# Optimization experiments

Hardware: AMD Instinct MI355X
Metric: run time of the kernel (lower is better)

The kernel has to match this reference:

```python
import jax, jax.numpy as jnp
import numpy as np

NUM_HEADS = 16
EPS = 1e-5


def setup_inputs() -> dict:
    key = jax.random.key(0)
    ks = jax.random.split(key, 9)
    B, S, D = 2, 2048, 1024
    s = 1.0 / np.sqrt(D)
    return {
        "x": jax.random.normal(ks[0], (B, S, D), dtype=jnp.float32),
        "Wq": jax.random.uniform(ks[1], (D, D), jnp.float32, -s, s),
        "bq": jax.random.uniform(ks[2], (D,), jnp.float32, -s, s),
        "Wk": jax.random.uniform(ks[3], (D, D), jnp.float32, -s, s),
        "bk": jax.random.uniform(ks[4], (D,), jnp.float32, -s, s),
        "Wv": jax.random.uniform(ks[5], (D, D), jnp.float32, -s, s),
        "bv": jax.random.uniform(ks[6], (D,), jnp.float32, -s, s),
        "Wo": jax.random.uniform(ks[7], (D, D), jnp.float32, -s, s),
        "bo": jax.random.uniform(ks[8], (D,), jnp.float32, -s, s),
    }


def reference(x, Wq, bq, Wk, bk, Wv, bv, Wo, bo):
    B, S, D = x.shape
    H = NUM_HEADS
    hd = D // H
    # projections -> [B, H, S, hd]
    def proj(W, b):
        return (x @ W + b).reshape(B, S, H, hd).transpose(0, 2, 1, 3)
    Q = proj(Wq, bq)
    K = proj(Wk, bk)
    V = proj(Wv, bv)
    scores = jnp.einsum("bhqd,bhkd->bhqk", Q, K) / jnp.sqrt(jnp.float32(hd))
    attn = jax.nn.softmax(scores, axis=-1)  # dropout is identity in eval mode
    out = jnp.einsum("bhqk,bhkd->bhqd", attn, V)
    out = out.transpose(0, 2, 1, 3).reshape(B, S, D)
    out = jax.nn.relu(out @ Wo + bo)
    mu = jnp.mean(out, axis=-1, keepdims=True)
    var = jnp.var(out, axis=-1, keepdims=True)
    return (out - mu) * jax.lax.rsqrt(var + EPS)
```

## Files before the change

kernel.cpp:

```cpp
#include <hip/hip_runtime.h>
#include <hip/hip_bf16.h>
#include <math.h>

#define Bb 2
#define Ss 2048
#define Dd 1024
#define Hh 16
#define HD 64
#define Mm (Bb*Ss)

typedef __attribute__((ext_vector_type(8))) short bf8_t;
typedef __attribute__((ext_vector_type(4))) float f4_t;
typedef __attribute__((ext_vector_type(4))) unsigned u4_t;
typedef __attribute__((ext_vector_type(2))) unsigned uint2v;

#define LOG2E 1.4426950408889634f

#define AS1 __attribute__((address_space(1)))
#define AS3 __attribute__((address_space(3)))

__device__ __forceinline__ void gl2lds16(const void* g, void* l) {
    __builtin_amdgcn_global_load_lds((const AS1 unsigned int*)g,
                                     (AS3 unsigned int*)l, 16, 0, 0);
}
__device__ __forceinline__ short bfr(float f) {
    __hip_bfloat16 h = __float2bfloat16(f);
    return *reinterpret_cast<short*>(&h);
}
__device__ __forceinline__ unsigned pkbf16(float a, float b) {
    const unsigned ua = __builtin_bit_cast(unsigned, a) + 0x8000u;
    const unsigned ub = __builtin_bit_cast(unsigned, b) + 0x8000u;
    return __builtin_amdgcn_perm(ub, ua, 0x07060302u);
}
__device__ __forceinline__ float fexp2(float x) {
    return __builtin_amdgcn_exp2f(x);
}
__device__ __forceinline__ float b2f(unsigned short u) {
    return __builtin_bit_cast(float, (unsigned)u << 16);
}
__device__ __forceinline__ void pl32(unsigned &a, unsigned &b) {
#if __has_builtin(__builtin_amdgcn_permlane32_swap)
    uint2v r = __builtin_amdgcn_permlane32_swap(a, b, false, false);
    a = r[0]; b = r[1];
#else
    asm volatile("v_permlane32_swap_b32 %0, %1" : "+v"(a), "+v"(b));
#endif
}
__device__ __forceinline__ void pl16(unsigned &a, unsigned &b) {
#if __has_builtin(__builtin_amdgcn_permlane16_swap)
    uint2v r = __builtin_amdgcn_permlane16_swap(a, b, false, false);
    a = r[0]; b = r[1];
#else
    asm volatile("v_permlane16_swap_b32 %0, %1" : "+v"(a), "+v"(b));
#endif
}

__global__ __launch_bounds__(256)
void prep(const float* __restrict__ x,
          const float* __restrict__ w0, const float* __restrict__ w1,
          const float* __restrict__ w2, const float* __restrict__ w3,
          __hip_bfloat16* __restrict__ Wt4, __hip_bfloat16* __restrict__ Xh)
{
    const int z = blockIdx.z;
    if (z < 4) {
        const float* W = (z == 0) ? w0 : (z == 1) ? w1 : (z == 2) ? w2 : w3;
        __hip_bfloat16* Wt = Wt4 + (size_t)z * Dd * Dd;
        __shared__ float t[32][33];
        const int n0 = blockIdx.x * 32, k0 = blockIdx.y * 32;
        const int tx = threadIdx.x & 31, ty = threadIdx.x >> 5;
        #pragma unroll
        for (int rr = 0; rr < 4; ++rr)
            t[ty + rr*8][tx] = W[(size_t)(k0 + ty + rr*8) * Dd + n0 + tx];
        __syncthreads();
        #pragma unroll
        for (int rr = 0; rr < 4; ++rr)
            Wt[(size_t)(n0 + ty + rr*8) * Dd + k0 + tx] =
                __float2bfloat16(t[tx][ty + rr*8]);
    } else {
        const int bid = (z - 4) * 1024 + blockIdx.y * 32 + blockIdx.x;
        const size_t i = ((size_t)bid * 256 + threadIdx.x) * 8;
        const float4 a = *(const float4*)&x[i];
        const float4 b = *(const float4*)&x[i + 4];
        bf8_t o;
        o[0] = bfr(a.x); o[1] = bfr(a.y); o[2] = bfr(a.z); o[3] = bfr(a.w);
        o[4] = bfr(b.x); o[5] = bfr(b.y); o[6] = bfr(b.z); o[7] = bfr(b.w);
        *(bf8_t*)&Xh[i] = o;
    }
}

__global__ __launch_bounds__(256)
void gemm_qkv(const __hip_bfloat16* __restrict__ A,
              const __hip_bfloat16* __restrict__ Bt,
              const float* __restrict__ b0, const float* __restrict__ b1,
              const float* __restrict__ b2,
              __hip_bfloat16* __restrict__ Qh, __hip_bfloat16* __restrict__ Kh,
              __hip_bfloat16* __restrict__ Vt)
{
    __shared__ __align__(16) char pool[34816];
    __hip_bfloat16* As = (__hip_bfloat16*)pool;
    __hip_bfloat16* Bs = As + 2 * 128 * 32;

    const int lin  = blockIdx.y * 24 + blockIdx.x;
    const int xcd  = lin & 7;
    const int idx  = lin >> 3;
    const int by   = (xcd >> 1) * 8 + idx / 12;
    const int bx   = (xcd & 1) * 12 + idx % 12;

    const int tid  = threadIdx.x;
    const int wave = tid >> 6;
    const int lane = tid & 63;
    const int llo  = lane & 15;
    const int lhi  = lane >> 4;
    const int wm   = wave & 1;
    const int wn   = wave >> 1;
    const int row0 = by * 128;
    const int col0 = bx * 128;

    size_t aoff[2], boff[2];
    int    loff[2];
    #pragma unroll
    for (int p = 0; p < 2; ++p) {
        const int g = p * 256 + wave * 64 + lane;
        const int r = g >> 2;
        const int kc = ((g & 3) ^ ((r >> 1) & 3)) * 8;
        aoff[p] = (size_t)(row0 + r) * Dd + kc;
        boff[p] = (size_t)(col0 + r) * Dd + kc;
        loff[p] = (p * 256 + wave * 64) * 16;
    }
    const __hip_bfloat16* Acur = A;
    const __hip_bfloat16* Bcur = Bt;

    auto stage = [&](int buf) {
        #pragma unroll
        for (int p = 0; p < 2; ++p) {
            gl2lds16(Acur + aoff[p], (char*)As + buf*8192 + loff[p]);
            gl2lds16(Bcur + boff[p], (char*)Bs + buf*8192 + loff[p]);
        }
        Acur += 32; Bcur += 32;
    };

    const int xch = (lhi ^ ((llo >> 1) & 3)) * 8;

    f4_t acc[4][4] = {};
    stage(0);
    for (int kt = 0; kt < 32; ++kt) {
        const int buf = kt & 1;
        __syncthreads();
        if (kt + 1 < 32) stage(buf ^ 1);

        bf8_t a[4], b[4];
        #pragma unroll
        for (int i = 0; i < 4; ++i)
            a[i] = *(const bf8_t*)&As[buf*4096 + (wm*64 + i*16 + llo) * 32 + xch];
        #pragma unroll
        for (int j = 0; j < 4; ++j)
            b[j] = *(const bf8_t*)&Bs[buf*4096 + (wn*64 + j*16 + llo) * 32 + xch];
        #pragma unroll
        for (int i = 0; i < 4; ++i)
            #pragma unroll
            for (int j = 0; j < 4; ++j)
                acc[i][j] = __builtin_amdgcn_mfma_f32_16x16x32_bf16(
                    a[i], b[j], acc[i][j], 0, 0, 0);
    }

    const int sel   = col0 >> 10;
    const int cbase = col0 & 1023;
    __hip_bfloat16* Ls = (__hip_bfloat16*)pool;
    __syncthreads();

    float bv[4];
    const float* bp = (sel == 0) ? b0 : (sel == 1) ? b1 : b2;
    #pragma unroll
    for (int j = 0; j < 4; ++j) bv[j] = bp[cbase + wn*64 + j*16 + llo];
    const float scale = (sel == 0) ? 0.125f * LOG2E : 1.0f;

    if (sel < 2) {
        #pragma unroll
        for (int i = 0; i < 4; ++i)
            #pragma unroll
            for (int r = 0; r < 4; ++r) {
                const int ml = wm*64 + i*16 + lhi*4 + r;
                #pragma unroll
                for (int j = 0; j < 4; ++j)
                    Ls[ml*136 + wn*64 + j*16 + llo] =
                        __float2bfloat16((acc[i][j][r] + bv[j]) * scale);
            }
        __syncthreads();
        __hip_bfloat16* outQK = (sel == 0) ? Qh : Kh;
        #pragma unroll
        for (int p = 0; p < 8; ++p) {
            const int id = p*256 + tid;
            const int rl = id >> 4;
            const int c8 = (id & 15) * 8;
            const bf8_t v = *(const bf8_t*)&Ls[rl*136 + c8];
            const int m  = row0 + rl;
            const int b_ = m >> 11, s_ = m & (Ss - 1);
            const int col = cbase + c8;
            *(bf8_t*)&outQK[((size_t)(b_*Hh + (col >> 6))*Ss + s_)*HD + (col & 63)] = v;
        }
    } else {
        #pragma unroll
        for (int i = 0; i < 4; ++i)
            #pragma unroll
            for (int r = 0; r < 4; ++r) {
                const int ml = wm*64 + i*16 + lhi*4 + r;
                #pragma unroll
                for (int j = 0; j < 4; ++j)
                    Ls[(wn*64 + j*16 + llo)*136 + ml] =
                        __float2bfloat16(acc[i][j][r] + bv[j]);
            }
        __syncthreads();
        const int b_ = row0 >> 11;
        const int sb = row0 & (Ss - 1);
        #pragma unroll
        for (int p = 0; p < 8; ++p) {
            const int cl = p*16 + (tid >> 4);
            const int m  = (tid & 15) * 8;
            const bf8_t v = *(const bf8_t*)&Ls[cl*136 + m];
            const int cc = cbase + cl;
            *(bf8_t*)&Vt[((size_t)(b_*Hh + (cc >> 6))*HD + (cc & 63))*Ss + sb + m] = v;
        }
    }
}

__global__ __launch_bounds__(256, 2)
void attn_mfma(const __hip_bfloat16* __restrict__ Qh,
               const __hip_bfloat16* __restrict__ Kh,
               const __hip_bfloat16* __restrict__ Vt,
               __hip_bfloat16* __restrict__ Ah)
{
    const int lin  = (blockIdx.z * Hh + blockIdx.y) * (Ss/128) + blockIdx.x;
    const int xcd  = lin & 7;
    const int slot = lin >> 3;
    const int grp  = (xcd << 2) | (slot >> 4);
    const int qc   = slot & 15;
    const int b    = grp >> 4;
    const int h    = grp & 15;

    const int wave = threadIdx.x >> 6;
    const int lane = threadIdx.x & 63;
    const int llo  = lane & 15;
    const int lhi  = lane >> 4;
    const int qb   = qc * 128 + wave * 32;

    const size_t base = ((size_t)(b*Hh + h)) * Ss * HD;

    __shared__ __hip_bfloat16 Ks[2][2 * 64 * 32];
    __shared__ __hip_bfloat16 Vs[2][2 * 64 * 32];

    int koff[2], voff[2], loff[2];
    #pragma unroll
    for (int it = 0; it < 2; ++it) {
        const int g  = it*256 + wave*64 + lane;
        const int hf = g >> 8;
        const int rr = (g >> 2) & 63;
        const int c8 = ((g & 3) ^ ((rr >> 1) & 3)) * 8;
        koff[it] = rr*HD + hf*32 + c8;
        voff[it] = rr*Ss + hf*32 + c8;
        loff[it] = (it*256 + wave*64) * 16;
    }
    const __hip_bfloat16* Kcur = Kh + base;
    const __hip_bfloat16* Vcur = Vt + base;

    auto stage = [&](int buf) {
        #pragma unroll
        for (int it = 0; it < 2; ++it) {
            gl2lds16(Kcur + koff[it], (char*)&Ks[buf][0] + loff[it]);
            gl2lds16(Vcur + voff[it], (char*)&Vs[buf][0] + loff[it]);
        }
        Kcur += 64 * HD;
        Vcur += 64;
    };

    bf8_t qf[2][2];
    #pragma unroll
    for (int s = 0; s < 2; ++s)
        #pragma unroll
        for (int d = 0; d < 2; ++d)
            qf[s][d] = *(const bf8_t*)&Qh[base + (size_t)(qb + 16*s + llo)*HD + 32*d + lhi*8];

    f4_t o_[2][4];
    f4_t lsum[2];
    #pragma unroll
    for (int s = 0; s < 2; ++s) {
        #pragma unroll
        for (int n = 0; n < 4; ++n) o_[s][n] = (f4_t){0.f,0.f,0.f,0.f};
        lsum[s] = (f4_t){0.f,0.f,0.f,0.f};
    }
    const short oneb = 0x3F80;
    const bf8_t vones = {oneb,oneb,oneb,oneb,oneb,oneb,oneb,oneb};

    const f4_t zf = {0.f,0.f,0.f,0.f};
    const int xch = (lhi ^ ((llo >> 1) & 3)) * 8;

    bf8_t pfp[2][2];
    bf8_t vfp[4][2];

    stage(0);

    for (int t = 0; t < Ss/64; ++t) {
        const int buf = t & 1;
        __syncthreads();
        if (t + 1 < Ss/64) stage(buf ^ 1);

        bf8_t kf[4][2];
        #pragma unroll
        for (int kc = 0; kc < 4; ++kc)
            #pragma unroll
            for (int d = 0; d < 2; ++d)
                kf[kc][d] = *(const bf8_t*)&Ks[buf][d*2048 + (kc*16 + llo)*32 + xch];

        f4_t sacc[2][4];
        #pragma unroll
        for (int s = 0; s < 2; ++s)
            #pragma unroll
            for (int kc = 0; kc < 4; ++kc) {
                sacc[s][kc] = __builtin_amdgcn_mfma_f32_16x16x32_bf16(kf[kc][0], qf[s][0], zf, 0, 0, 0);
                sacc[s][kc] = __builtin_amdgcn_mfma_f32_16x16x32_bf16(kf[kc][1], qf[s][1], sacc[s][kc], 0, 0, 0);
            }

        if (t > 0) {
            __builtin_amdgcn_s_setprio(1);
            #pragma unroll
            for (int d = 0; d < 2; ++d)
                #pragma unroll
                for (int nc = 0; nc < 4; ++nc)
                    #pragma unroll
                    for (int s = 0; s < 2; ++s)
                        o_[s][nc] = __builtin_amdgcn_mfma_f32_16x16x32_bf16(pfp[s][d], vfp[nc][d], o_[s][nc], 0, 0, 0);
            #pragma unroll
            for (int s = 0; s < 2; ++s)
                #pragma unroll
                for (int d = 0; d < 2; ++d)
                    lsum[s] = __builtin_amdgcn_mfma_f32_16x16x32_bf16(pfp[s][d], vones, lsum[s], 0, 0, 0);
            __builtin_amdgcn_s_setprio(0);
        }

        #pragma unroll
        for (int nc = 0; nc < 4; ++nc)
            #pragma unroll
            for (int d = 0; d < 2; ++d)
                vfp[nc][d] = *(const bf8_t*)&Vs[buf][d*2048 + (nc*16 + llo)*32 + xch];

        #pragma unroll
        for (int s = 0; s < 2; ++s) {
            unsigned w[4][2];
            #pragma unroll
            for (int kc = 0; kc < 4; ++kc) {
                const float p0 = fexp2(sacc[s][kc][0]);
                const float p1 = fexp2(sacc[s][kc][1]);
                const float p2 = fexp2(sacc[s][kc][2]);
                const float p3 = fexp2(sacc[s][kc][3]);
                w[kc][0] = pkbf16(p0, p1);
                w[kc][1] = pkbf16(p2, p3);
            }
            #pragma unroll
            for (int d = 0; d < 2; ++d) {
                u4_t pu;
                #pragma unroll
                for (int hh = 0; hh < 2; ++hh) {
                    unsigned U = w[2*d][hh], V = w[2*d+1][hh];
                    pl32(U, V);
                    pl16(U, V);
                    pu[hh]     = U;
                    pu[2 + hh] = V;
                }
                pfp[s][d] = __builtin_bit_cast(bf8_t, pu);
            }
        }
    }

    #pragma unroll
    for (int d = 0; d < 2; ++d)
        #pragma unroll
        for (int nc = 0; nc < 4; ++nc)
            #pragma unroll
            for (int s = 0; s < 2; ++s)
                o_[s][nc] = __builtin_amdgcn_mfma_f32_16x16x32_bf16(pfp[s][d], vfp[nc][d], o_[s][nc], 0, 0, 0);
    #pragma unroll
    for (int s = 0; s < 2; ++s)
        #pragma unroll
        for (int d = 0; d < 2; ++d)
            lsum[s] = __builtin_amdgcn_mfma_f32_16x16x32_bf16(pfp[s][d], vones, lsum[s], 0, 0, 0);

    #pragma unroll
    for (int s = 0; s < 2; ++s) {
        #pragma unroll
        for (int r = 0; r < 4; ++r) {
            const float inv = 1.0f / lsum[s][r];
            const int q = qb + 16*s + 4*lhi + r;
            __hip_bfloat16* orow = &Ah[((size_t)(b*Ss) + q)*Dd + h*HD + llo];
            #pragma unroll
            for (int nc = 0; nc < 4; ++nc)
                orow[16*nc] = __float2bfloat16(o_[s][nc][r] * inv);
        }
    }
}

__global__ __launch_bounds__(256)
void gemm_out(const __hip_bfloat16* __restrict__ A,
              const __hip_bfloat16* __restrict__ Bt,
              __hip_bfloat16* __restrict__ Ro)
{
    __shared__ __hip_bfloat16 As[2][128 * 32];
    __shared__ __hip_bfloat16 Bs[2][128 * 32];

    const int lin  = (blockIdx.z * 32 + blockIdx.y) * 8 + blockIdx.x;
    const int nlin = (lin & 7) * 64 + (lin >> 3);
    const int bx   = nlin & 7;
    const int rest = nlin >> 3;
    const int by   = rest & 31;
    const int z    = rest >> 5;

    const int tid  = threadIdx.x;
    const int wave = tid >> 6;
    const int lane = tid & 63;
    const int llo  = lane & 15;
    const int lhi  = lane >> 4;
    const int wm   = wave & 1;
    const int wn   = wave >> 1;
    const int row0 = by * 128;
    const int col0 = bx * 128;

    size_t aoff[2], boff[2];
    int    loff[2];
    #pragma unroll
    for (int p = 0; p < 2; ++p) {
        const int g = p * 256 + wave * 64 + lane;
        const int r = g >> 2;
        const int kc = ((g & 3) ^ ((r >> 1) & 3)) * 8;
        aoff[p] = (size_t)(row0 + r) * Dd + kc;
        boff[p] = (size_t)(col0 + r) * Dd + kc;
        loff[p] = (p * 256 + wave * 64) * 16;
    }
    const __hip_bfloat16* Acur = A  + (size_t)z * (Dd/2);
    const __hip_bfloat16* Bcur = Bt + (size_t)z * (Dd/2);

    auto stage = [&](int buf) {
        #pragma unroll
        for (int p = 0; p < 2; ++p) {
            gl2lds16(Acur + aoff[p], (char*)&As[buf][0] + loff[p]);
            gl2lds16(Bcur + boff[p], (char*)&Bs[buf][0] + loff[p]);
        }
        Acur += 32; Bcur += 32;
    };

    const int xch = (lhi ^ ((llo >> 1) & 3)) * 8;

    f4_t acc[4][4] = {};
    stage(0);
    for (int kt = 0; kt < 16; ++kt) {
        const int buf = kt & 1;
        __syncthreads();
        if (kt + 1 < 16) stage(buf ^ 1);

        bf8_t a[4], b[4];
        #pragma unroll
        for (int i = 0; i < 4; ++i)
            a[i] = *(const bf8_t*)&As[buf][(wm*64 + i*16 + llo) * 32 + xch];
        #pragma unroll
        for (int j = 0; j < 4; ++j)
            b[j] = *(const bf8_t*)&Bs[buf][(wn*64 + j*16 + llo) * 32 + xch];
        #pragma unroll
        for (int i = 0; i < 4; ++i)
            #pragma unroll
            for (int j = 0; j < 4; ++j)
                acc[i][j] = __builtin_amdgcn_mfma_f32_16x16x32_bf16(
                    a[i], b[j], acc[i][j], 0, 0, 0);
    }

    __hip_bfloat16* Roz = Ro + (size_t)z * Mm * Dd;
    #pragma unroll
    for (int i = 0; i < 4; ++i) {
        #pragma unroll
        for (int r = 0; r < 4; ++r) {
            const int m = row0 + wm*64 + i*16 + lhi*4 + r;
            #pragma unroll
            for (int j = 0; j < 4; ++j) {
                const int col = col0 + wn*64 + j*16 + llo;
                Roz[(size_t)m * Dd + col] = __float2bfloat16(acc[i][j][r]);
            }
        }
    }
}

__global__ __launch_bounds__(256)
void layernorm(const __hip_bfloat16* __restrict__ P0,
               const __hip_bfloat16* __restrict__ P1,
               const float* __restrict__ bias, float* __restrict__ out)
{
    const int row = blockIdx.x;
    const int c = threadIdx.x;
    const ushort4 a = ((const ushort4*)(P0 + (size_t)row*Dd))[c];
    const ushort4 b = ((const ushort4*)(P1 + (size_t)row*Dd))[c];
    const float4 bb = ((const float4*)bias)[c];
    float4 v;
    v.x = fmaxf(b2f(a.x) + b2f(b.x) + bb.x, 0.0f);
    v.y = fmaxf(b2f(a.y) + b2f(b.y) + bb.y, 0.0f);
    v.z = fmaxf(b2f(a.z) + b2f(b.z) + bb.z, 0.0f);
    v.w = fmaxf(b2f(a.w) + b2f(b.w) + bb.w, 0.0f);

    float s  = v.x + v.y + v.z + v.w;
    float ss = v.x*v.x + v.y*v.y + v.z*v.z + v.w*v.w;
    #pragma unroll
    for (int off = 32; off > 0; off >>= 1) {
        s  += __shfl_down(s,  off);
        ss += __shfl_down(ss, off);
    }
    __shared__ float rs[4], rss[4];
    const int wid = c >> 6, lid = c & 63;
    if (lid == 0) { rs[wid] = s; rss[wid] = ss; }
    __syncthreads();
    s  = rs[0] + rs[1] + rs[2] + rs[3];
    ss = rss[0] + rss[1] + rss[2] + rss[3];
    const float mean = s * (1.0f / Dd);
    const float var  = ss * (1.0f / Dd) - mean * mean;
    const float rstd = rsqrtf(var + 1e-5f);
    float4 o;
    o.x = (v.x - mean) * rstd;
    o.y = (v.y - mean) * rstd;
    o.z = (v.z - mean) * rstd;
    o.w = (v.w - mean) * rstd;
    ((float4*)(out + (size_t)row*Dd))[c] = o;
}

extern "C" void kernel_launch(void* const* d_in, const int* in_sizes, int n_in,
                              void* d_out, int out_size, void* d_ws, size_t ws_size,
                              hipStream_t stream)
{
    const float* x  = (const float*)d_in[0];
    const float* Wq = (const float*)d_in[1];
    const float* bq = (const float*)d_in[2];
    const float* Wk = (const float*)d_in[3];
    const float* bk = (const float*)d_in[4];
    const float* Wv = (const float*)d_in[5];
    const float* bv = (const float*)d_in[6];
    const float* Wo = (const float*)d_in[7];
    const float* bo = (const float*)d_in[8];
    float* out = (float*)d_out;

    __hip_bfloat16* Xh    = (__hip_bfloat16*)d_ws;
    __hip_bfloat16* Wqkvt = Xh    + (size_t)Mm*Dd;
    __hip_bfloat16* Wot   = Wqkvt + (size_t)3*Dd*Dd;
    __hip_bfloat16* Ah    = Wot   + (size_t)Dd*Dd;
    __hip_bfloat16* Qh    = Ah    + (size_t)Mm*Dd;
    __hip_bfloat16* Kh    = Qh    + (size_t)Mm*Dd;
    __hip_bfloat16* Vt    = Kh    + (size_t)Mm*Dd;
    __hip_bfloat16* Rb    = Qh;

    prep<<<dim3(32, 32, 6), dim3(256), 0, stream>>>(x, Wq, Wk, Wv, Wo, Wqkvt, Xh);
    gemm_qkv<<<dim3(3*Dd/128, Mm/128), dim3(256), 0, stream>>>(
        Xh, Wqkvt, bq, bk, bv, Qh, Kh, Vt);
    attn_mfma<<<dim3(Ss/128, Hh, Bb), dim3(256), 0, stream>>>(Qh, Kh, Vt, Ah);
    gemm_out<<<dim3(Dd/128, Mm/128, 2), dim3(256), 0, stream>>>(Ah, Wot, Rb);
    layernorm<<<dim3(Mm), dim3(256), 0, stream>>>(Rb, Rb + (size_t)Mm*Dd, bo, out);
}
```

Baseline: 190.1 us.

## Replace split-K output GEMM with full-K 128x64 tiles and fused bias+ReLU epilogue

```diff
diff --git a/kernel.cpp b/kernel.cpp
--- a/kernel.cpp
+++ b/kernel.cpp
@@ -400,17 +400,18 @@
 __global__ __launch_bounds__(256)
 void gemm_out(const __hip_bfloat16* __restrict__ A,
               const __hip_bfloat16* __restrict__ Bt,
-              __hip_bfloat16* __restrict__ Ro)
+              const float* __restrict__ bias,
+              __hip_bfloat16* __restrict__ R)
 {
-    __shared__ __hip_bfloat16 As[2][128 * 32];
-    __shared__ __hip_bfloat16 Bs[2][128 * 32];
-
-    const int lin  = (blockIdx.z * 32 + blockIdx.y) * 8 + blockIdx.x;
-    const int nlin = (lin & 7) * 64 + (lin >> 3);
-    const int bx   = nlin & 7;
-    const int rest = nlin >> 3;
-    const int by   = rest & 31;
-    const int z    = rest >> 5;
+    __shared__ __align__(16) char pool[24576];
+    __hip_bfloat16* As = (__hip_bfloat16*)pool;
+    __hip_bfloat16* Bs = As + 2 * 128 * 32;
+
+    const int lin = blockIdx.y * 16 + blockIdx.x;
+    const int xcd = lin & 7;
+    const int idx = lin >> 3;
+    const int by  = (xcd >> 1) * 8 + (idx >> 3);
+    const int bx  = (xcd & 1) * 8 + (idx & 7);
 
     const int tid  = threadIdx.x;
     const int wave = tid >> 6;
@@ -420,85 +421,96 @@
     const int wm   = wave & 1;
     const int wn   = wave >> 1;
     const int row0 = by * 128;
-    const int col0 = bx * 128;
-
-    size_t aoff[2], boff[2];
-    int    loff[2];
+    const int col0 = bx * 64;
+
+    size_t aoff[2], boff;
+    int    loffA[2], loffB;
     #pragma unroll
     for (int p = 0; p < 2; ++p) {
         const int g = p * 256 + wave * 64 + lane;
         const int r = g >> 2;
         const int kc = ((g & 3) ^ ((r >> 1) & 3)) * 8;
-        aoff[p] = (size_t)(row0 + r) * Dd + kc;
-        boff[p] = (size_t)(col0 + r) * Dd + kc;
-        loff[p] = (p * 256 + wave * 64) * 16;
-    }
-    const __hip_bfloat16* Acur = A  + (size_t)z * (Dd/2);
-    const __hip_bfloat16* Bcur = Bt + (size_t)z * (Dd/2);
+        aoff[p]  = (size_t)(row0 + r) * Dd + kc;
+        loffA[p] = (p * 256 + wave * 64) * 16;
+    }
+    {
+        const int g = wave * 64 + lane;
+        const int r = g >> 2;
+        const int kc = ((g & 3) ^ ((r >> 1) & 3)) * 8;
+        boff  = (size_t)(col0 + r) * Dd + kc;
+        loffB = (wave * 64) * 16;
+    }
+    const __hip_bfloat16* Acur = A;
+    const __hip_bfloat16* Bcur = Bt;
 
     auto stage = [&](int buf) {
         #pragma unroll
-        for (int p = 0; p < 2; ++p) {
-            gl2lds16(Acur + aoff[p], (char*)&As[buf][0] + loff[p]);
-            gl2lds16(Bcur + boff[p], (char*)&Bs[buf][0] + loff[p]);
-        }
+        for (int p = 0; p < 2; ++p)
+            gl2lds16(Acur + aoff[p], (char*)As + buf*8192 + loffA[p]);
+        gl2lds16(Bcur + boff, (char*)Bs + buf*4096 + loffB);
         Acur += 32; Bcur += 32;
     };
 
     const int xch = (lhi ^ ((llo >> 1) & 3)) * 8;
 
-    f4_t acc[4][4] = {};
+    f4_t acc[4][2] = {};
     stage(0);
-    for (int kt = 0; kt < 16; ++kt) {
+    for (int kt = 0; kt < 32; ++kt) {
         const int buf = kt & 1;
         __syncthreads();
-        if (kt + 1 < 16) stage(buf ^ 1);
-
-        bf8_t a[4], b[4];
+        if (kt + 1 < 32) stage(buf ^ 1);
+
+        bf8_t a[4], b[2];
         #pragma unroll
         for (int i = 0; i < 4; ++i)
-            a[i] = *(const bf8_t*)&As[buf][(wm*64 + i*16 + llo) * 32 + xch];
-        #pragma unroll
-        for (int j = 0; j < 4; ++j)
-            b[j] = *(const bf8_t*)&Bs[buf][(wn*64 + j*16 + llo) * 32 + xch];
+            a[i] = *(const bf8_t*)&As[buf*4096 + (wm*64 + i*16 + llo) * 32 + xch];
+        #pragma unroll
+        for (int j = 0; j < 2; ++j)
+            b[j] = *(const bf8_t*)&Bs[buf*2048 + (wn*32 + j*16 + llo) * 32 + xch];
         #pragma unroll
         for (int i = 0; i < 4; ++i)
             #pragma unroll
-            for (int j = 0; j < 4; ++j)
+            for (int j = 0; j < 2; ++j)
                 acc[i][j] = __builtin_amdgcn_mfma_f32_16x16x32_bf16(
                     a[i], b[j], acc[i][j], 0, 0, 0);
     }
 
-    __hip_bfloat16* Roz = Ro + (size_t)z * Mm * Dd;
-    #pragma unroll
-    for (int i = 0; i < 4; ++i) {
+    __hip_bfloat16* Ls = (__hip_bfloat16*)pool;
+    __syncthreads();
+
+    float bv[2];
+    #pragma unroll
+    for (int j = 0; j < 2; ++j) bv[j] = bias[col0 + wn*32 + j*16 + llo];
+
+    #pragma unroll
+    for (int i = 0; i < 4; ++i)
         #pragma unroll
         for (int r = 0; r < 4; ++r) {
-            const int m = row0 + wm*64 + i*16 + lhi*4 + r;
-            #pragma unroll
-            for (int j = 0; j < 4; ++j) {
-                const int col = col0 + wn*64 + j*16 + llo;
-                Roz[(size_t)m * Dd + col] = __float2bfloat16(acc[i][j][r]);
-            }
-        }
+            const int ml = wm*64 + i*16 + lhi*4 + r;
+            #pragma unroll
+            for (int j = 0; j < 2; ++j)
+                Ls[ml*72 + wn*32 + j*16 + llo] =
+                    __float2bfloat16(fmaxf(acc[i][j][r] + bv[j], 0.0f));
+        }
+    __syncthreads();
+    #pragma unroll
+    for (int p = 0; p < 4; ++p) {
+        const int id = p*256 + tid;
+        const int rl = id >> 3;
+        const int c8 = (id & 7) * 8;
+        const bf8_t v = *(const bf8_t*)&Ls[rl*72 + c8];
+        *(bf8_t*)&R[(size_t)(row0 + rl)*Dd + col0 + c8] = v;
     }
 }
 
 __global__ __launch_bounds__(256)
-void layernorm(const __hip_bfloat16* __restrict__ P0,
-               const __hip_bfloat16* __restrict__ P1,
-               const float* __restrict__ bias, float* __restrict__ out)
+void layernorm(const __hip_bfloat16* __restrict__ R, float* __restrict__ out)
 {
     const int row = blockIdx.x;
     const int c = threadIdx.x;
-    const ushort4 a = ((const ushort4*)(P0 + (size_t)row*Dd))[c];
-    const ushort4 b = ((const ushort4*)(P1 + (size_t)row*Dd))[c];
-    const float4 bb = ((const float4*)bias)[c];
+    const ushort4 a = ((const ushort4*)(R + (size_t)row*Dd))[c];
     float4 v;
-    v.x = fmaxf(b2f(a.x) + b2f(b.x) + bb.x, 0.0f);
-    v.y = fmaxf(b2f(a.y) + b2f(b.y) + bb.y, 0.0f);
-    v.z = fmaxf(b2f(a.z) + b2f(b.z) + bb.z, 0.0f);
-    v.w = fmaxf(b2f(a.w) + b2f(b.w) + bb.w, 0.0f);
+    v.x = b2f(a.x); v.y = b2f(a.y); v.z = b2f(a.z); v.w = b2f(a.w);
 
     float s  = v.x + v.y + v.z + v.w;
     float ss = v.x*v.x + v.y*v.y + v.z*v.z + v.w*v.w;
@@ -552,6 +564,6 @@
     gemm_qkv<<<dim3(3*Dd/128, Mm/128), dim3(256), 0, stream>>>(
         Xh, Wqkvt, bq, bk, bv, Qh, Kh, Vt);
     attn_mfma<<<dim3(Ss/128, Hh, Bb), dim3(256), 0, stream>>>(Qh, Kh, Vt, Ah);
-    gemm_out<<<dim3(Dd/128, Mm/128, 2), dim3(256), 0, stream>>>(Ah, Wot, Rb);
-    layernorm<<<dim3(Mm), dim3(256), 0, stream>>>(Rb, Rb + (size_t)Mm*Dd, bo, out);
-}
+    gemm_out<<<dim3(Dd/64, Mm/128), dim3(256), 0, stream>>>(Ah, Wot, bo, Rb);
+    layernorm<<<dim3(Mm), dim3(256), 0, stream>>>(Rb, out);
+}
```

Measured after the change: 189.1 us. About the same (-0.5%).
